# Optimization experiments

Hardware: AMD Instinct MI355X
Metric: run time of the kernel (lower is better)

Reference implementation:

```python
import jax, jax.numpy as jnp
import numpy as np

N = 8192        # nodes
E = 262144      # edges (avg degree 32)
IN_CH = 256
CH = 128
SLOPE = 0.2     # PyG GATv2Conv default negative_slope


def gatv2(x, src, dst, wl, wr, att, b):
    """Single-head GATv2Conv (PyG defaults: share_weights=False, self-loops
    already appended to src/dst). x: [N, in]; wl, wr: [out, in]; att: [out]."""
    xl = x @ wl.T                      # [N, out] source-side transform (x_j)
    xr = x @ wr.T                      # [N, out] target-side transform (x_i)
    # per-edge attention logit: att . LeakyReLU(x_l[src] + x_r[dst])
    e = jax.nn.leaky_relu(xl[src] + xr[dst], SLOPE) @ att   # [E']
    # segment softmax over incoming edges of each target node
    m = jax.ops.segment_max(e, dst, num_segments=N)
    p = jnp.exp(e - m[dst])
    s = jax.ops.segment_sum(p, dst, num_segments=N)
    alpha = p / s[dst]                 # every node has a self-loop -> s > 0
    out = jax.ops.segment_sum(alpha[:, None] * xl[src], dst, num_segments=N)
    return out + b


def setup_inputs() -> dict:
    key = jax.random.key(0)
    ks = jax.random.split(key, 2 + 5 * 3)
    inp = {
        "x": jax.random.normal(ks[0], (N, IN_CH), dtype=jnp.float32),
        "edge_index": jax.random.randint(ks[1], (2, E), 0, N, dtype=jnp.int64),
    }
    dims = [(CH, IN_CH), (2 * CH, CH), (CH, 2 * CH), (CH, 2 * CH), (IN_CH, CH)]
    ki = 2
    for i, (oc, ic) in enumerate(dims, start=1):
        sc = (2.0 / (ic + oc)) ** 0.5  # glorot-ish
        inp[f"w{i}l"] = jax.random.normal(ks[ki], (oc, ic), dtype=jnp.float32) * sc
        inp[f"w{i}r"] = jax.random.normal(ks[ki + 1], (oc, ic), dtype=jnp.float32) * sc
        inp[f"a{i}"] = jax.random.normal(ks[ki + 2], (oc,), dtype=jnp.float32) * sc
        inp[f"b{i}"] = jnp.zeros((oc,), dtype=jnp.float32)
        ki += 3
    return inp


def reference(x, edge_index,
              w1l, w1r, a1, b1,
              w2l, w2r, a2, b2,
              w3l, w3r, a3, b3,
              w4l, w4r, a4, b4,
              w5l, w5r, a5, b5):
    loops = jnp.arange(N, dtype=edge_index.dtype)
    src = jnp.concatenate([edge_index[0], loops])   # add_self_loops=True
    dst = jnp.concatenate([edge_index[1], loops])
    h = jax.nn.relu(gatv2(x, src, dst, w1l, w1r, a1, b1))          # [N, CH]
    z = jax.nn.relu(gatv2(h, src, dst, w2l, w2r, a2, b2))          # [N, 2CH]
    re = jax.nn.relu(gatv2(z, src, dst, w3l, w3r, a3, b3))         # [N, CH]
    recon_edge = jax.nn.sigmoid(re @ re.T)                         # [N, N]
    xd = jax.nn.relu(gatv2(z, src, dst, w4l, w4r, a4, b4))         # [N, CH]
    x_rec = jax.nn.relu(gatv2(xd, src, dst, w5l, w5r, a5, b5))     # [N, IN_CH]
    return recon_edge, x_rec, z
```

## Files before the change

### kernel.cpp

```cpp
#include <hip/hip_runtime.h>
#include <hip/hip_bf16.h>
#include <math.h>

#define N_NODES 8192
#define N_EDGES 262144
#define EP (N_EDGES + N_NODES)
#define SLOPE 0.2f

typedef short bf16x8 __attribute__((ext_vector_type(8)));
typedef short short4v __attribute__((ext_vector_type(4)));
typedef unsigned short u16x8 __attribute__((ext_vector_type(8)));
typedef float f32x4 __attribute__((ext_vector_type(4)));

__global__ void extract_hist(const int* __restrict__ raw,
                             int* __restrict__ esrc, int* __restrict__ edst,
                             int* __restrict__ counts) {
    __shared__ int sflag;
    int t = threadIdx.x;
    if (t < 64) {
        unsigned long long b = __ballot(raw[2 * t + 1] != 0);
        if (t == 0) sflag = (b == 0ULL) ? 1 : 0;
    }
    __syncthreads();
    int i64f = sflag;
    int k = blockIdx.x * blockDim.x + t;
    if (k >= N_EDGES) return;
    int s, d;
    if (i64f) {
        s = raw[2 * (size_t)k];
        d = raw[2 * ((size_t)N_EDGES + k)];
    } else {
        s = raw[k];
        d = raw[N_EDGES + k];
    }
    esrc[k] = s;
    edst[k] = d;
    atomicAdd(&counts[d], 1);
}

__global__ void scan_k(const int* __restrict__ counts, int* __restrict__ row_ptr) {
    __shared__ int part[256];
    int t = threadIdx.x;
    int base = t * 32;
    int loc[32];
    int s = 0;
    for (int i = 0; i < 32; ++i) { loc[i] = s; s += counts[base + i] + 1; }
    part[t] = s;
    __syncthreads();
    for (int off = 1; off < 256; off <<= 1) {
        int tmp = (t >= off) ? part[t - off] : 0;
        __syncthreads();
        part[t] += tmp;
        __syncthreads();
    }
    int incl = part[t];
    int excl = incl - s;
    for (int i = 0; i < 32; ++i) row_ptr[base + i] = excl + loc[i];
    if (t == 255) row_ptr[N_NODES] = incl;
}

__global__ void scatter_k(const int* __restrict__ esrc, const int* __restrict__ edst,
                          const int* __restrict__ row_ptr, int* __restrict__ cursor,
                          int* __restrict__ ssrc) {
    int k = blockIdx.x * blockDim.x + threadIdx.x;
    if (k >= EP) return;
    int s, d;
    if (k < N_EDGES) { s = esrc[k]; d = edst[k]; }
    else             { s = d = k - N_EDGES; }
    int pos = row_ptr[d] + atomicAdd(&cursor[d], 1);
    ssrc[pos] = s;
}

struct WPrep {
    const float* wl[5];
    const float* wr[5];
    int oc[5];
    int lk[5];
};

__global__ void prep_all(WPrep P, const float* __restrict__ x,
                         short* __restrict__ W3all, short* __restrict__ A3) {
    int gid = blockIdx.x * blockDim.x + threadIdx.x;
    if (gid < 524288) {
        int r = gid >> 6;
        int c4 = (gid & 63) << 2;
        f32x4 a = *(const f32x4*)&x[((size_t)r << 8) + c4];
        short4v h4, l4;
#pragma unroll
        for (int j = 0; j < 4; ++j) {
            __hip_bfloat16 hb = __float2bfloat16(a[j]);
            float hf = __bfloat162float(hb);
            __hip_bfloat16 lb = __float2bfloat16(a[j] - hf);
            h4[j] = *(short*)&hb;
            l4[j] = *(short*)&lb;
        }
        size_t ro = (size_t)r * 768;
        *(short4v*)&A3[ro + c4] = h4;
        *(short4v*)&A3[ro + 256 + c4] = l4;
        *(short4v*)&A3[ro + 512 + c4] = h4;
    } else {
        int g = gid - 524288;
        int l = g >> 16;
        if (l >= 5) return;
        int rem = g & 65535;
        int lk = P.lk[l], K = 1 << lk;
        int r = rem >> lk, c = rem & (K - 1);
        int OC = P.oc[l];
        const float* w = (r < OC) ? P.wl[l] : P.wr[l];
        int rr = (r < OC) ? r : r - OC;
        float a = w[((size_t)rr << lk) + c];
        __hip_bfloat16 hb = __float2bfloat16(a);
        float hf = __bfloat162float(hb);
        __hip_bfloat16 lb = __float2bfloat16(a - hf);
        size_t ro = (size_t)l * 196608 + (size_t)r * 3 * K;
        W3all[ro + c] = *(short*)&hb;
        W3all[ro + K + c] = *(short*)&hb;
        W3all[ro + 2 * K + c] = *(short*)&lb;
    }
}

#if __has_builtin(__builtin_amdgcn_global_load_lds)
#define GL16(gsrc, lbase, lofs)                                                       \
    __builtin_amdgcn_global_load_lds((const __attribute__((address_space(1))) void*)(gsrc), \
                                     (__attribute__((address_space(3))) void*)(lbase), 16, 0, 0)
#else
#define GL16(gsrc, lbase, lofs) (*(bf16x8*)((lbase) + (lofs)) = *(const bf16x8*)(gsrc))
#endif

__global__ __launch_bounds__(256) void gemm_bf16_nt(const short* __restrict__ A3,
                                                    const short* __restrict__ W3,
                                                    unsigned short* __restrict__ XLb,
                                                    float* __restrict__ XRf,
                                                    int K3, int N2, int ocl, int lgpl) {
    __shared__ __align__(16) short As[2][4096];
    __shared__ __align__(16) short Bs[2][4096];
    int tid = threadIdx.x;
    int gx = gridDim.x;
    int lgx = (gx == 8) ? 3 : 2;
    int orig = blockIdx.x + (blockIdx.y << lgx);
    int nwg = gx << 7;
    int swzb = (orig & 7) * (nwg >> 3) + (orig >> 3);
    int bx = swzb & (gx - 1), by = swzb >> lgx;
    int i0 = by * 64, j0 = bx * 64;

    int wave = tid >> 6, lane = tid & 63;
    int b0 = wave * 1024 + lane * 16;
    int row0 = b0 >> 7;
    int rb0 = b0 & 127;
    int scb = rb0 ^ ((row0 & 7) << 4);
    const short* gA0 = A3 + (size_t)(i0 + row0) * K3 + (scb >> 1);
    const short* gA1 = A3 + (size_t)(i0 + row0 + 32) * K3 + (scb >> 1);
    const short* gB0 = W3 + (size_t)(j0 + row0) * K3 + (scb >> 1);
    const short* gB1 = W3 + (size_t)(j0 + row0 + 32) * K3 + (scb >> 1);
    int lofs = lane * 8;

#define STAGE(pb, k0s)                                      \
    do {                                                    \
        GL16(gA0 + (k0s), &As[pb][wave * 512], lofs);       \
        GL16(gA1 + (k0s), &As[pb][2048 + wave * 512], lofs);\
        GL16(gB0 + (k0s), &Bs[pb][wave * 512], lofs);       \
        GL16(gB1 + (k0s), &Bs[pb][2048 + wave * 512], lofs);\
    } while (0)

    int wr = (wave >> 1) * 32, wc = (wave & 1) * 32;
    int lm = lane & 15, quad = lane >> 4;
    f32x4 acc[2][2] = {};
    int nt = K3 >> 6;
    STAGE(0, 0);
    int cur = 0;
    for (int t = 0; t < nt; ++t) {
        if (t + 1 < nt) {
            STAGE(cur ^ 1, (t + 1) << 6);
            asm volatile("s_waitcnt vmcnt(4)" ::: "memory");
        } else {
            asm volatile("s_waitcnt vmcnt(0)" ::: "memory");
        }
        __builtin_amdgcn_s_barrier();
        __builtin_amdgcn_sched_barrier(0);
        const char* Ab = (const char*)&As[cur][0];
        const char* Bb = (const char*)&Bs[cur][0];
#pragma unroll
        for (int ks = 0; ks < 2; ++ks) {
            int kb = ks * 64 + quad * 16;
            bf16x8 a[2], b[2];
#pragma unroll
            for (int u = 0; u < 2; ++u) {
                int r = wr + u * 16 + lm;
                a[u] = *(const bf16x8*)(Ab + (((r << 7) | kb) ^ ((r & 7) << 4)));
            }
#pragma unroll
            for (int v = 0; v < 2; ++v) {
                int r = wc + v * 16 + lm;
                b[v] = *(const bf16x8*)(Bb + (((r << 7) | kb) ^ ((r & 7) << 4)));
            }
#pragma unroll
            for (int u = 0; u < 2; ++u)
#pragma unroll
                for (int v = 0; v < 2; ++v)
                    acc[u][v] = __builtin_amdgcn_mfma_f32_16x16x32_bf16(a[u], b[v], acc[u][v], 0, 0, 0);
        }
        __builtin_amdgcn_sched_barrier(0);
        __builtin_amdgcn_s_barrier();
        cur ^= 1;
    }
#undef STAGE
    int plm = (1 << lgpl) - 1;
#pragma unroll
    for (int u = 0; u < 2; ++u)
#pragma unroll
        for (int v = 0; v < 2; ++v)
#pragma unroll
            for (int r = 0; r < 4; ++r) {
                int row = i0 + wr + u * 16 + quad * 4 + r;
                int col = j0 + wc + v * 16 + lm;
                int slab = col >> lgpl;
                int wn = col & plm;
                float val = acc[u][v][r];
                size_t base = (size_t)slab * N_NODES * ocl + (size_t)row * ocl;
                if (wn < ocl) {
                    __hip_bfloat16 hb = __float2bfloat16(val);
                    XLb[base + wn] = *(unsigned short*)&hb;
                } else {
                    XRf[base + wn - ocl] = val;
                }
            }
}

#define LSTR 136

__global__ __launch_bounds__(256) void recon_sym(const unsigned short* __restrict__ Rb,
                                                 float* __restrict__ C) {
    __shared__ __align__(16) short Sh[2 * 128 * LSTR];
    short* As = Sh;
    short* Bs = Sh + 128 * LSTR;
    int tid = threadIdx.x;
    int orig = blockIdx.x;
    int s = (orig & 7) * 260 + (orig >> 3);
    float ff = 64.5f - sqrtf(64.5f * 64.5f - 2.0f * (float)s);
    int bi = (int)ff;
    while (bi > 0 && 64 * bi - bi * (bi - 1) / 2 > s) --bi;
    while (64 * (bi + 1) - (bi + 1) * bi / 2 <= s) ++bi;
    int bj = bi + (s - (64 * bi - bi * (bi - 1) / 2));
    int i0 = bi * 128, j0 = bj * 128;
    const short* R = (const short*)Rb;
#pragma unroll
    for (int c = 0; c < 8; ++c) {
        int idx = tid + c * 256;
        int row = idx >> 4, col = (idx & 15) * 8;
        *(bf16x8*)(&As[row * LSTR + col]) = *(const bf16x8*)(&R[(size_t)(i0 + row) * 128 + col]);
        *(bf16x8*)(&Bs[row * LSTR + col]) = *(const bf16x8*)(&R[(size_t)(j0 + row) * 128 + col]);
    }
    __syncthreads();
    int wave = tid >> 6, lane = tid & 63;
    int wr = (wave >> 1) * 64, wc = (wave & 1) * 64;
    int lm = lane & 15, quad = lane >> 4;
    f32x4 acc[4][4] = {};
#pragma unroll
    for (int ks = 0; ks < 4; ++ks) {
        int ko = ks * 32 + quad * 8;
        bf16x8 a[4], b[4];
#pragma unroll
        for (int u = 0; u < 4; ++u)
            a[u] = *(const bf16x8*)(&As[(wr + u * 16 + lm) * LSTR + ko]);
#pragma unroll
        for (int v = 0; v < 4; ++v)
            b[v] = *(const bf16x8*)(&Bs[(wc + v * 16 + lm) * LSTR + ko]);
#pragma unroll
        for (int u = 0; u < 4; ++u)
#pragma unroll
            for (int v = 0; v < 4; ++v)
                acc[u][v] = __builtin_amdgcn_mfma_f32_16x16x32_bf16(a[u], b[v], acc[u][v], 0, 0, 0);
    }
#pragma unroll
    for (int u = 0; u < 4; ++u)
#pragma unroll
        for (int v = 0; v < 4; ++v)
#pragma unroll
            for (int r = 0; r < 4; ++r) {
                acc[u][v][r] = 1.0f / (1.0f + __expf(-acc[u][v][r]));
                int row = i0 + wr + u * 16 + quad * 4 + r;
                int col = j0 + wc + v * 16 + lm;
                C[(size_t)row * 8192 + col] = acc[u][v][r];
            }
    if (bi != bj) {
        __syncthreads();
        float* T = (float*)Sh;
#pragma unroll
        for (int u = 0; u < 4; ++u)
#pragma unroll
            for (int v = 0; v < 4; ++v)
#pragma unroll
                for (int r = 0; r < 4; ++r)
                    T[(wr + u * 16 + quad * 4 + r) * 129 + (wc + v * 16 + lm)] = acc[u][v][r];
        __syncthreads();
#pragma unroll
        for (int it = 0; it < 64; ++it) {
            int idx = tid + it * 256;
            int rp = idx >> 7, cp = idx & 127;
            C[(size_t)(j0 + rp) * 8192 + (i0 + cp)] = T[cp * 129 + rp];
        }
    }
}

struct GatP {
    const float* att; const float* bias;
    float* outf; short* a3; unsigned short* rb;
    const unsigned short* xlb; const float* xrf;
};

__device__ __forceinline__ void cvt8(u16x8 w, float* v) {
#pragma unroll
    for (int j = 0; j < 8; ++j) v[j] = __uint_as_float(((unsigned)w[j]) << 16);
}

__global__ __launch_bounds__(256) void gat128(const int* __restrict__ row_ptr,
                                              const int* __restrict__ ssrc,
                                              GatP P0, GatP P1) {
    __shared__ float sacc[16][128];
    __shared__ float ss[16];
    int d = blockIdx.x & (N_NODES - 1);
    GatP P = (blockIdx.x >= N_NODES) ? P1 : P0;
    int t = threadIdx.x, ln = t & 15, g = t >> 4;
    int beg = row_ptr[d], end = row_ptr[d + 1];
    float xr[8], at[8];
    {
        f32x4 a0 = *(const f32x4*)&P.xrf[(size_t)d * 128 + ln * 8];
        f32x4 a1 = *(const f32x4*)&P.xrf[(size_t)d * 128 + ln * 8 + 4];
        f32x4 b0 = *(const f32x4*)&P.att[ln * 8];
        f32x4 b1 = *(const f32x4*)&P.att[ln * 8 + 4];
#pragma unroll
        for (int j = 0; j < 4; ++j) { xr[j] = a0[j]; xr[4 + j] = a1[j]; at[j] = b0[j]; at[4 + j] = b1[j]; }
    }
    float s = 0.0f, acc[8] = {};
    int p = beg + g;
    for (; p + 16 < end; p += 32) {
        int s0 = ssrc[p], s1 = ssrc[p + 16];
        float v0[8], v1[8];
        cvt8(*(const u16x8*)&P.xlb[(size_t)s0 * 128 + ln * 8], v0);
        cvt8(*(const u16x8*)&P.xlb[(size_t)s1 * 128 + ln * 8], v1);
        float e0 = 0.0f, e1 = 0.0f;
#pragma unroll
        for (int j = 0; j < 8; ++j) {
            float u0 = v0[j] + xr[j]; u0 = (u0 > 0.0f) ? u0 : SLOPE * u0; e0 += u0 * at[j];
            float u1 = v1[j] + xr[j]; u1 = (u1 > 0.0f) ? u1 : SLOPE * u1; e1 += u1 * at[j];
        }
#pragma unroll
        for (int off = 8; off; off >>= 1) {
            e0 += __shfl_xor(e0, off, 64);
            e1 += __shfl_xor(e1, off, 64);
        }
        float q0 = __expf(e0), q1 = __expf(e1);
        s += q0 + q1;
#pragma unroll
        for (int j = 0; j < 8; ++j) acc[j] += q0 * v0[j] + q1 * v1[j];
    }
    if (p < end) {
        int si = ssrc[p];
        float v[8];
        cvt8(*(const u16x8*)&P.xlb[(size_t)si * 128 + ln * 8], v);
        float e = 0.0f;
#pragma unroll
        for (int j = 0; j < 8; ++j) {
            float u = v[j] + xr[j];
            u = (u > 0.0f) ? u : SLOPE * u;
            e += u * at[j];
        }
#pragma unroll
        for (int off = 8; off; off >>= 1) e += __shfl_xor(e, off, 64);
        float q = __expf(e);
        s += q;
#pragma unroll
        for (int j = 0; j < 8; ++j) acc[j] += q * v[j];
    }
#pragma unroll
    for (int j = 0; j < 8; ++j) sacc[g][ln * 8 + j] = acc[j];
    if (ln == 0) ss[g] = s;
    __syncthreads();
    if (t < 128) {
        float tot = 0.0f, st = 0.0f;
#pragma unroll
        for (int w = 0; w < 16; ++w) { tot += sacc[w][t]; st += ss[w]; }
        float val = fmaxf(tot / st + P.bias[t], 0.0f);
        if (P.outf) P.outf[(size_t)d * 128 + t] = val;
        if (P.a3) {
            __hip_bfloat16 hb = __float2bfloat16(val);
            float hf = __bfloat162float(hb);
            __hip_bfloat16 lb = __float2bfloat16(val - hf);
            size_t ro = (size_t)d * 384;
            P.a3[ro + t] = *(short*)&hb;
            P.a3[ro + 128 + t] = *(short*)&lb;
            P.a3[ro + 256 + t] = *(short*)&hb;
        }
        if (P.rb) {
            __hip_bfloat16 hb = __float2bfloat16(val);
            P.rb[d * 128 + t] = *(unsigned short*)&hb;
        }
    }
}

__global__ __launch_bounds__(256) void gat256(const int* __restrict__ row_ptr,
                                              const int* __restrict__ ssrc,
                                              const unsigned short* __restrict__ xlb,
                                              const float* __restrict__ xrf,
                                              const float* __restrict__ att,
                                              const float* __restrict__ bias,
                                              float* __restrict__ outf,
                                              short* __restrict__ a3) {
    __shared__ float sacc[8][256];
    __shared__ float ss[8];
    int d = blockIdx.x, t = threadIdx.x;
    int ln = t & 31, g = t >> 5;
    int beg = row_ptr[d], end = row_ptr[d + 1];
    float xr[8], at[8];
    {
        f32x4 a0 = *(const f32x4*)&xrf[(size_t)d * 256 + ln * 8];
        f32x4 a1 = *(const f32x4*)&xrf[(size_t)d * 256 + ln * 8 + 4];
        f32x4 b0 = *(const f32x4*)&att[ln * 8];
        f32x4 b1 = *(const f32x4*)&att[ln * 8 + 4];
#pragma unroll
        for (int j = 0; j < 4; ++j) { xr[j] = a0[j]; xr[4 + j] = a1[j]; at[j] = b0[j]; at[4 + j] = b1[j]; }
    }
    float s = 0.0f, acc[8] = {};
    int p = beg + g;
    for (; p + 8 < end; p += 16) {
        int s0 = ssrc[p], s1 = ssrc[p + 8];
        float v0[8], v1[8];
        cvt8(*(const u16x8*)&xlb[(size_t)s0 * 256 + ln * 8], v0);
        cvt8(*(const u16x8*)&xlb[(size_t)s1 * 256 + ln * 8], v1);
        float e0 = 0.0f, e1 = 0.0f;
#pragma unroll
        for (int j = 0; j < 8; ++j) {
            float u0 = v0[j] + xr[j]; u0 = (u0 > 0.0f) ? u0 : SLOPE * u0; e0 += u0 * at[j];
            float u1 = v1[j] + xr[j]; u1 = (u1 > 0.0f) ? u1 : SLOPE * u1; e1 += u1 * at[j];
        }
#pragma unroll
        for (int off = 16; off; off >>= 1) {
            e0 += __shfl_xor(e0, off, 64);
            e1 += __shfl_xor(e1, off, 64);
        }
        float q0 = __expf(e0), q1 = __expf(e1);
        s += q0 + q1;
#pragma unroll
        for (int j = 0; j < 8; ++j) acc[j] += q0 * v0[j] + q1 * v1[j];
    }
    if (p < end) {
        int si = ssrc[p];
        float v[8];
        cvt8(*(const u16x8*)&xlb[(size_t)si * 256 + ln * 8], v);
        float e = 0.0f;
#pragma unroll
        for (int j = 0; j < 8; ++j) {
            float u = v[j] + xr[j];
            u = (u > 0.0f) ? u : SLOPE * u;
            e += u * at[j];
        }
#pragma unroll
        for (int off = 16; off; off >>= 1) e += __shfl_xor(e, off, 64);
        float q = __expf(e);
        s += q;
#pragma unroll
        for (int j = 0; j < 8; ++j) acc[j] += q * v[j];
    }
#pragma unroll
    for (int j = 0; j < 8; ++j) sacc[g][ln * 8 + j] = acc[j];
    if (ln == 0) ss[g] = s;
    __syncthreads();
    {
        float tot = 0.0f, st = 0.0f;
#pragma unroll
        for (int w = 0; w < 8; ++w) { tot += sacc[w][t]; st += ss[w]; }
        float val = fmaxf(tot / st + bias[t], 0.0f);
        if (outf) outf[(size_t)d * 256 + t] = val;
        if (a3) {
            __hip_bfloat16 hb = __float2bfloat16(val);
            float hf = __bfloat162float(hb);
            __hip_bfloat16 lb = __float2bfloat16(val - hf);
            size_t ro = (size_t)d * 768;
            a3[ro + t] = *(short*)&hb;
            a3[ro + 256 + t] = *(short*)&lb;
            a3[ro + 512 + t] = *(short*)&hb;
        }
    }
}

static inline int ceil_div(int a, int b) { return (a + b - 1) / b; }

extern "C" void kernel_launch(void* const* d_in, const int* in_sizes, int n_in,
                              void* d_out, int out_size, void* d_ws, size_t ws_size,
                              hipStream_t stream) {
    const float* x    = (const float*)d_in[0];
    const int*   eraw = (const int*)d_in[1];

    WPrep P;
    const float* att[5];
    const float* bia[5];
    for (int l = 0; l < 5; ++l) {
        P.wl[l] = (const float*)d_in[2 + 4 * l + 0];
        P.wr[l] = (const float*)d_in[2 + 4 * l + 1];
        att[l]  = (const float*)d_in[2 + 4 * l + 2];
        bia[l]  = (const float*)d_in[2 + 4 * l + 3];
    }
    const int och[5]  = {128, 256, 128, 128, 256};
    const int logK[5] = {8, 7, 8, 8, 7};
    for (int l = 0; l < 5; ++l) { P.oc[l] = och[l]; P.lk[l] = logK[l]; }

    float* outp  = (float*)d_out;
    float* recon = outp;
    float* xrec  = outp + (size_t)67108864;
    float* zout  = outp + (size_t)69206016;

    float* W = (float*)d_ws;
    unsigned short* XLb = (unsigned short*)W;
    float* XRf   = W + 1048576;
    short* A3    = (short*)(W + 3145728);
    short* W3all = (short*)(W + 6291456);
    unsigned short* Rb = (unsigned short*)(W + 6782976);
    int* I       = (int*)(W + 7307264);
    int* counts  = I;
    int* cursor  = I + 8192;
    int* row_ptr = I + 16384;
    int* ssrc    = I + 24577;
    int* esrc    = I + 294913;
    int* edst    = I + 557057;

    hipMemsetAsync(counts, 0, 2 * 8192 * sizeof(int), stream);
    extract_hist<<<ceil_div(N_EDGES, 256), 256, 0, stream>>>(eraw, esrc, edst, counts);
    scan_k<<<1, 256, 0, stream>>>(counts, row_ptr);
    scatter_k<<<ceil_div(EP, 256), 256, 0, stream>>>(esrc, edst, row_ptr, cursor, ssrc);

    prep_all<<<3328, 256, 0, stream>>>(P, x, W3all, A3);

    {
        dim3 g(4, 128);
        gemm_bf16_nt<<<g, 256, 0, stream>>>(A3, W3all + 0 * 196608, XLb, XRf, 768, 256, 128, 8);
        GatP g0{att[0], bia[0], nullptr, A3, nullptr, XLb, XRf};
        gat128<<<N_NODES, 256, 0, stream>>>(row_ptr, ssrc, g0, g0);
    }
    {
        dim3 g(8, 128);
        gemm_bf16_nt<<<g, 256, 0, stream>>>(A3, W3all + 1 * 196608, XLb, XRf, 384, 512, 256, 9);
        gat256<<<N_NODES, 256, 0, stream>>>(row_ptr, ssrc, XLb, XRf, att[1], bia[1], zout, A3);
    }
    {
        dim3 g(8, 128);
        gemm_bf16_nt<<<g, 256, 0, stream>>>(A3, W3all + 2 * 196608, XLb, XRf, 768, 512, 128, 8);
        GatP g2{att[2], bia[2], nullptr, nullptr, Rb, XLb, XRf};
        GatP g3{att[3], bia[3], nullptr, A3, nullptr, XLb + (size_t)N_NODES * 128, XRf + (size_t)N_NODES * 128};
        gat128<<<2 * N_NODES, 256, 0, stream>>>(row_ptr, ssrc, g2, g3);
        recon_sym<<<2080, 256, 0, stream>>>(Rb, recon);
    }
    {
        dim3 g(8, 128);
        gemm_bf16_nt<<<g, 256, 0, stream>>>(A3, W3all + 4 * 196608, XLb, XRf, 384, 512, 256, 9);
        gat256<<<N_NODES, 256, 0, stream>>>(row_ptr, ssrc, XLb, XRf, att[4], bia[4], xrec, nullptr);
    }
}
```

Measured before the change: 521.7 us.

## Split recon GEMM into 64-tiles and co-schedule with last-layer GEMM and GAT

The symmetric recon_edge GEMM is rebuilt with 64x64 tiles (8256 upper-triangle tiles) and split into two halves. One half is appended as extra blocks to the layer-5 projection GEMM and the other to the layer-5 GAT kernel, so the store-bound recon work overlaps with those small kernels instead of running alone. Edge histogramming is also folded into the weight/input prep kernel, the separate esrc/edst extraction pass is removed (scatter reads the raw indices), scan stages counts in LDS, and recon stores become nontemporal. The cost is more tile-index arithmetic, larger shared memory per block, and possible load imbalance between heterogeneous blocks.

```diff
diff --git a/kernel.cpp b/kernel.cpp
--- a/kernel.cpp
+++ b/kernel.cpp
@@ -11,65 +11,6 @@
 typedef short short4v __attribute__((ext_vector_type(4)));
 typedef unsigned short u16x8 __attribute__((ext_vector_type(8)));
 typedef float f32x4 __attribute__((ext_vector_type(4)));
-
-__global__ void extract_hist(const int* __restrict__ raw,
-                             int* __restrict__ esrc, int* __restrict__ edst,
-                             int* __restrict__ counts) {
-    __shared__ int sflag;
-    int t = threadIdx.x;
-    if (t < 64) {
-        unsigned long long b = __ballot(raw[2 * t + 1] != 0);
-        if (t == 0) sflag = (b == 0ULL) ? 1 : 0;
-    }
-    __syncthreads();
-    int i64f = sflag;
-    int k = blockIdx.x * blockDim.x + t;
-    if (k >= N_EDGES) return;
-    int s, d;
-    if (i64f) {
-        s = raw[2 * (size_t)k];
-        d = raw[2 * ((size_t)N_EDGES + k)];
-    } else {
-        s = raw[k];
-        d = raw[N_EDGES + k];
-    }
-    esrc[k] = s;
-    edst[k] = d;
-    atomicAdd(&counts[d], 1);
-}
-
-__global__ void scan_k(const int* __restrict__ counts, int* __restrict__ row_ptr) {
-    __shared__ int part[256];
-    int t = threadIdx.x;
-    int base = t * 32;
-    int loc[32];
-    int s = 0;
-    for (int i = 0; i < 32; ++i) { loc[i] = s; s += counts[base + i] + 1; }
-    part[t] = s;
-    __syncthreads();
-    for (int off = 1; off < 256; off <<= 1) {
-        int tmp = (t >= off) ? part[t - off] : 0;
-        __syncthreads();
-        part[t] += tmp;
-        __syncthreads();
-    }
-    int incl = part[t];
-    int excl = incl - s;
-    for (int i = 0; i < 32; ++i) row_ptr[base + i] = excl + loc[i];
-    if (t == 255) row_ptr[N_NODES] = incl;
-}
-
-__global__ void scatter_k(const int* __restrict__ esrc, const int* __restrict__ edst,
-                          const int* __restrict__ row_ptr, int* __restrict__ cursor,
-                          int* __restrict__ ssrc) {
-    int k = blockIdx.x * blockDim.x + threadIdx.x;
-    if (k >= EP) return;
-    int s, d;
-    if (k < N_EDGES) { s = esrc[k]; d = edst[k]; }
-    else             { s = d = k - N_EDGES; }
-    int pos = row_ptr[d] + atomicAdd(&cursor[d], 1);
-    ssrc[pos] = s;
-}
 
 struct WPrep {
     const float* wl[5];
@@ -78,8 +19,10 @@
     int lk[5];
 };
 
-__global__ void prep_all(WPrep P, const float* __restrict__ x,
-                         short* __restrict__ W3all, short* __restrict__ A3) {
+__global__ void prologue(WPrep P, const float* __restrict__ x,
+                         short* __restrict__ W3all, short* __restrict__ A3,
+                         const int* __restrict__ raw, int* __restrict__ counts) {
+    __shared__ int sflag;
     int gid = blockIdx.x * blockDim.x + threadIdx.x;
     if (gid < 524288) {
         int r = gid >> 6;
@@ -98,10 +41,9 @@
         *(short4v*)&A3[ro + c4] = h4;
         *(short4v*)&A3[ro + 256 + c4] = l4;
         *(short4v*)&A3[ro + 512 + c4] = h4;
-    } else {
+    } else if (gid < 851968) {
         int g = gid - 524288;
         int l = g >> 16;
-        if (l >= 5) return;
         int rem = g & 65535;
         int lk = P.lk[l], K = 1 << lk;
         int r = rem >> lk, c = rem & (K - 1);
@@ -116,7 +58,61 @@
         W3all[ro + c] = *(short*)&hb;
         W3all[ro + K + c] = *(short*)&hb;
         W3all[ro + 2 * K + c] = *(short*)&lb;
-    }
+    } else {
+        int t = threadIdx.x;
+        if (t < 64) {
+            unsigned long long b = __ballot(raw[2 * t + 1] != 0);
+            if (t == 0) sflag = (b == 0ULL) ? 1 : 0;
+        }
+        __syncthreads();
+        int k = gid - 851968;
+        int d = sflag ? raw[2 * ((size_t)N_EDGES + k)] : raw[N_EDGES + k];
+        atomicAdd(&counts[d], 1);
+    }
+}
+
+__global__ void scan_k(const int* __restrict__ counts, int* __restrict__ row_ptr) {
+    __shared__ int buf[8192];
+    __shared__ int part[256];
+    int t = threadIdx.x;
+    for (int i = 0; i < 32; ++i) buf[i * 256 + t] = counts[i * 256 + t];
+    __syncthreads();
+    int base = t * 32;
+    int loc[32];
+    int s = 0;
+    for (int i = 0; i < 32; ++i) { loc[i] = s; s += buf[base + i] + 1; }
+    part[t] = s;
+    __syncthreads();
+    for (int off = 1; off < 256; off <<= 1) {
+        int tmp = (t >= off) ? part[t - off] : 0;
+        __syncthreads();
+        part[t] += tmp;
+        __syncthreads();
+    }
+    int incl = part[t];
+    int excl = incl - s;
+    for (int i = 0; i < 32; ++i) row_ptr[base + i] = excl + loc[i];
+    if (t == 255) row_ptr[N_NODES] = incl;
+}
+
+__global__ void scatter_k(const int* __restrict__ raw, const int* __restrict__ row_ptr,
+                          int* __restrict__ cursor, int* __restrict__ ssrc) {
+    __shared__ int sflag;
+    int t = threadIdx.x;
+    if (t < 64) {
+        unsigned long long b = __ballot(raw[2 * t + 1] != 0);
+        if (t == 0) sflag = (b == 0ULL) ? 1 : 0;
+    }
+    __syncthreads();
+    int k = blockIdx.x * blockDim.x + t;
+    if (k >= EP) return;
+    int s, d;
+    if (k < N_EDGES) {
+        if (sflag) { s = raw[2 * (size_t)k]; d = raw[2 * ((size_t)N_EDGES + k)]; }
+        else       { s = raw[k]; d = raw[N_EDGES + k]; }
+    } else s = d = k - N_EDGES;
+    int pos = row_ptr[d] + atomicAdd(&cursor[d], 1);
+    ssrc[pos] = s;
 }
 
 #if __has_builtin(__builtin_amdgcn_global_load_lds)
@@ -127,22 +123,12 @@
 #define GL16(gsrc, lbase, lofs) (*(bf16x8*)((lbase) + (lofs)) = *(const bf16x8*)(gsrc))
 #endif
 
-__global__ __launch_bounds__(256) void gemm_bf16_nt(const short* __restrict__ A3,
-                                                    const short* __restrict__ W3,
-                                                    unsigned short* __restrict__ XLb,
-                                                    float* __restrict__ XRf,
-                                                    int K3, int N2, int ocl, int lgpl) {
-    __shared__ __align__(16) short As[2][4096];
-    __shared__ __align__(16) short Bs[2][4096];
+__device__ __forceinline__ void gemm_body(const short* __restrict__ A3, const short* __restrict__ W3,
+                                          unsigned short* __restrict__ XLb, float* __restrict__ XRf,
+                                          int K3, int ocl, int lgpl,
+                                          int bx, int by, short* SH) {
     int tid = threadIdx.x;
-    int gx = gridDim.x;
-    int lgx = (gx == 8) ? 3 : 2;
-    int orig = blockIdx.x + (blockIdx.y << lgx);
-    int nwg = gx << 7;
-    int swzb = (orig & 7) * (nwg >> 3) + (orig >> 3);
-    int bx = swzb & (gx - 1), by = swzb >> lgx;
     int i0 = by * 64, j0 = bx * 64;
-
     int wave = tid >> 6, lane = tid & 63;
     int b0 = wave * 1024 + lane * 16;
     int row0 = b0 >> 7;
@@ -156,10 +142,12 @@
 
 #define STAGE(pb, k0s)                                      \
     do {                                                    \
-        GL16(gA0 + (k0s), &As[pb][wave * 512], lofs);       \
-        GL16(gA1 + (k0s), &As[pb][2048 + wave * 512], lofs);\
-        GL16(gB0 + (k0s), &Bs[pb][wave * 512], lofs);       \
-        GL16(gB1 + (k0s), &Bs[pb][2048 + wave * 512], lofs);\
+        short* Ad = SH + (pb) * 4096;                       \
+        short* Bd = SH + 8192 + (pb) * 4096;                \
+        GL16(gA0 + (k0s), Ad + wave * 512, lofs);           \
+        GL16(gA1 + (k0s), Ad + 2048 + wave * 512, lofs);    \
+        GL16(gB0 + (k0s), Bd + wave * 512, lofs);           \
+        GL16(gB1 + (k0s), Bd + 2048 + wave * 512, lofs);    \
     } while (0)
 
     int wr = (wave >> 1) * 32, wc = (wave & 1) * 32;
@@ -177,8 +165,8 @@
         }
         __builtin_amdgcn_s_barrier();
         __builtin_amdgcn_sched_barrier(0);
-        const char* Ab = (const char*)&As[cur][0];
-        const char* Bb = (const char*)&Bs[cur][0];
+        const char* Ab = (const char*)(SH + cur * 4096);
+        const char* Bb = (const char*)(SH + 8192 + cur * 4096);
 #pragma unroll
         for (int ks = 0; ks < 2; ++ks) {
             int kb = ks * 64 + quad * 16;
@@ -226,79 +214,109 @@
             }
 }
 
-#define LSTR 136
-
-__global__ __launch_bounds__(256) void recon_sym(const unsigned short* __restrict__ Rb,
-                                                 float* __restrict__ C) {
-    __shared__ __align__(16) short Sh[2 * 128 * LSTR];
-    short* As = Sh;
-    short* Bs = Sh + 128 * LSTR;
+__global__ __launch_bounds__(256) void gemm_std(const short* __restrict__ A3,
+                                                const short* __restrict__ W3,
+                                                unsigned short* __restrict__ XLb,
+                                                float* __restrict__ XRf,
+                                                int K3, int ocl, int lgpl, int lgx) {
+    __shared__ __align__(16) short SH[16384];
+    int nwg = gridDim.x;
+    int orig = blockIdx.x;
+    int swzb = (orig & 7) * (nwg >> 3) + (orig >> 3);
+    int bx = swzb & ((1 << lgx) - 1), by = swzb >> lgx;
+    gemm_body(A3, W3, XLb, XRf, K3, ocl, lgpl, bx, by, SH);
+}
+
+__device__ __forceinline__ void recon64_body(int s, const unsigned short* __restrict__ Rb,
+                                             float* __restrict__ C, short* SH) {
+    float ff = 128.5f - sqrtf(128.5f * 128.5f - 2.0f * (float)s);
+    int bi = (int)ff;
+    if (bi < 0) bi = 0;
+    if (bi > 127) bi = 127;
+    while (bi > 0 && (bi * (257 - bi)) / 2 > s) --bi;
+    while (((bi + 1) * (257 - (bi + 1))) / 2 <= s) ++bi;
+    int bj = bi + (s - (bi * (257 - bi)) / 2);
+    int i0 = bi * 64, j0 = bj * 64;
+    short* As = SH;
+    short* Bs = SH + 64 * 136;
+    const short* R = (const short*)Rb;
     int tid = threadIdx.x;
-    int orig = blockIdx.x;
-    int s = (orig & 7) * 260 + (orig >> 3);
-    float ff = 64.5f - sqrtf(64.5f * 64.5f - 2.0f * (float)s);
-    int bi = (int)ff;
-    while (bi > 0 && 64 * bi - bi * (bi - 1) / 2 > s) --bi;
-    while (64 * (bi + 1) - (bi + 1) * bi / 2 <= s) ++bi;
-    int bj = bi + (s - (64 * bi - bi * (bi - 1) / 2));
-    int i0 = bi * 128, j0 = bj * 128;
-    const short* R = (const short*)Rb;
-#pragma unroll
-    for (int c = 0; c < 8; ++c) {
+#pragma unroll
+    for (int c = 0; c < 4; ++c) {
         int idx = tid + c * 256;
         int row = idx >> 4, col = (idx & 15) * 8;
-        *(bf16x8*)(&As[row * LSTR + col]) = *(const bf16x8*)(&R[(size_t)(i0 + row) * 128 + col]);
-        *(bf16x8*)(&Bs[row * LSTR + col]) = *(const bf16x8*)(&R[(size_t)(j0 + row) * 128 + col]);
+        *(bf16x8*)(&As[row * 136 + col]) = *(const bf16x8*)(&R[(size_t)(i0 + row) * 128 + col]);
+        *(bf16x8*)(&Bs[row * 136 + col]) = *(const bf16x8*)(&R[(size_t)(j0 + row) * 128 + col]);
     }
     __syncthreads();
     int wave = tid >> 6, lane = tid & 63;
-    int wr = (wave >> 1) * 64, wc = (wave & 1) * 64;
+    int wr = (wave >> 1) * 32, wc = (wave & 1) * 32;
     int lm = lane & 15, quad = lane >> 4;
-    f32x4 acc[4][4] = {};
+    f32x4 acc[2][2] = {};
 #pragma unroll
     for (int ks = 0; ks < 4; ++ks) {
         int ko = ks * 32 + quad * 8;
-        bf16x8 a[4], b[4];
-#pragma unroll
-        for (int u = 0; u < 4; ++u)
-            a[u] = *(const bf16x8*)(&As[(wr + u * 16 + lm) * LSTR + ko]);
-#pragma unroll
-        for (int v = 0; v < 4; ++v)
-            b[v] = *(const bf16x8*)(&Bs[(wc + v * 16 + lm) * LSTR + ko]);
-#pragma unroll
-        for (int u = 0; u < 4; ++u)
-#pragma unroll
-            for (int v = 0; v < 4; ++v)
+        bf16x8 a[2], b[2];
+#pragma unroll
+        for (int u = 0; u < 2; ++u)
+            a[u] = *(const bf16x8*)(&As[(wr + u * 16 + lm) * 136 + ko]);
+#pragma unroll
+        for (int v = 0; v < 2; ++v)
+            b[v] = *(const bf16x8*)(&Bs[(wc + v * 16 + lm) * 136 + ko]);
+#pragma unroll
+        for (int u = 0; u < 2; ++u)
+#pragma unroll
+            for (int v = 0; v < 2; ++v)
                 acc[u][v] = __builtin_amdgcn_mfma_f32_16x16x32_bf16(a[u], b[v], acc[u][v], 0, 0, 0);
     }
 #pragma unroll
-    for (int u = 0; u < 4; ++u)
-#pragma unroll
-        for (int v = 0; v < 4; ++v)
+    for (int u = 0; u < 2; ++u)
+#pragma unroll
+        for (int v = 0; v < 2; ++v)
 #pragma unroll
             for (int r = 0; r < 4; ++r) {
-                acc[u][v][r] = 1.0f / (1.0f + __expf(-acc[u][v][r]));
+                float sg = 1.0f / (1.0f + __expf(-acc[u][v][r]));
+                acc[u][v][r] = sg;
                 int row = i0 + wr + u * 16 + quad * 4 + r;
                 int col = j0 + wc + v * 16 + lm;
-                C[(size_t)row * 8192 + col] = acc[u][v][r];
+                __builtin_nontemporal_store(sg, &C[(size_t)row * 8192 + col]);
             }
     if (bi != bj) {
         __syncthreads();
-        float* T = (float*)Sh;
-#pragma unroll
-        for (int u = 0; u < 4; ++u)
-#pragma unroll
-            for (int v = 0; v < 4; ++v)
+        float* T = (float*)SH;
+#pragma unroll
+        for (int u = 0; u < 2; ++u)
+#pragma unroll
+            for (int v = 0; v < 2; ++v)
 #pragma unroll
                 for (int r = 0; r < 4; ++r)
-                    T[(wr + u * 16 + quad * 4 + r) * 129 + (wc + v * 16 + lm)] = acc[u][v][r];
+                    T[(wr + u * 16 + quad * 4 + r) * 65 + (wc + v * 16 + lm)] = acc[u][v][r];
         __syncthreads();
 #pragma unroll
-        for (int it = 0; it < 64; ++it) {
+        for (int it = 0; it < 16; ++it) {
             int idx = tid + it * 256;
-            int rp = idx >> 7, cp = idx & 127;
-            C[(size_t)(j0 + rp) * 8192 + (i0 + cp)] = T[cp * 129 + rp];
-        }
+            int rp = idx >> 6, cp = idx & 63;
+            __builtin_nontemporal_store(T[cp * 65 + rp], &C[(size_t)(j0 + rp) * 8192 + (i0 + cp)]);
+        }
+    }
+}
+
+__global__ __launch_bounds__(256) void gemm_recon(const short* __restrict__ A3,
+                                                  const short* __restrict__ W3,
+                                                  unsigned short* __restrict__ XLb,
+                                                  float* __restrict__ XRf,
+                                                  int K3, int ocl, int lgpl,
+                                                  const unsigned short* __restrict__ Rb,
+                                                  float* __restrict__ C, int sbase) {
+    __shared__ __align__(16) short SH[17408];
+    int id = blockIdx.x;
+    if (id < 1024) {
+        int swzb = (id & 7) * 128 + (id >> 3);
+        gemm_body(A3, W3, XLb, XRf, K3, ocl, lgpl, swzb & 7, swzb >> 3, SH);
+    } else {
+        int orig = id - 1024;
+        int s = (orig & 7) * 516 + (orig >> 3) + sbase;
+        recon64_body(s, Rb, C, SH);
     }
 }
 
@@ -398,17 +416,16 @@
     }
 }
 
-__global__ __launch_bounds__(256) void gat256(const int* __restrict__ row_ptr,
-                                              const int* __restrict__ ssrc,
-                                              const unsigned short* __restrict__ xlb,
-                                              const float* __restrict__ xrf,
-                                              const float* __restrict__ att,
-                                              const float* __restrict__ bias,
-                                              float* __restrict__ outf,
-                                              short* __restrict__ a3) {
-    __shared__ float sacc[8][256];
-    __shared__ float ss[8];
-    int d = blockIdx.x, t = threadIdx.x;
+__device__ __forceinline__ void gat256_body(const int* __restrict__ row_ptr,
+                                            const int* __restrict__ ssrc,
+                                            const unsigned short* __restrict__ xlb,
+                                            const float* __restrict__ xrf,
+                                            const float* __restrict__ att,
+                                            const float* __restrict__ bias,
+                                            float* __restrict__ outf,
+                                            short* __restrict__ a3,
+                                            int d, float* sacc, float* ss) {
+    int t = threadIdx.x;
     int ln = t & 31, g = t >> 5;
     int beg = row_ptr[d], end = row_ptr[d + 1];
     float xr[8], at[8];
@@ -462,13 +479,13 @@
         for (int j = 0; j < 8; ++j) acc[j] += q * v[j];
     }
 #pragma unroll
-    for (int j = 0; j < 8; ++j) sacc[g][ln * 8 + j] = acc[j];
+    for (int j = 0; j < 8; ++j) sacc[g * 256 + ln * 8 + j] = acc[j];
     if (ln == 0) ss[g] = s;
     __syncthreads();
     {
         float tot = 0.0f, st = 0.0f;
 #pragma unroll
-        for (int w = 0; w < 8; ++w) { tot += sacc[w][t]; st += ss[w]; }
+        for (int w = 0; w < 8; ++w) { tot += sacc[w * 256 + t]; st += ss[w]; }
         float val = fmaxf(tot / st + bias[t], 0.0f);
         if (outf) outf[(size_t)d * 256 + t] = val;
         if (a3) {
@@ -480,6 +497,39 @@
             a3[ro + 256 + t] = *(short*)&lb;
             a3[ro + 512 + t] = *(short*)&hb;
         }
+    }
+}
+
+__global__ __launch_bounds__(256) void gat256(const int* __restrict__ row_ptr,
+                                              const int* __restrict__ ssrc,
+                                              const unsigned short* __restrict__ xlb,
+                                              const float* __restrict__ xrf,
+                                              const float* __restrict__ att,
+                                              const float* __restrict__ bias,
+                                              float* __restrict__ outf,
+                                              short* __restrict__ a3) {
+    __shared__ float SA[8 * 256 + 8];
+    gat256_body(row_ptr, ssrc, xlb, xrf, att, bias, outf, a3, blockIdx.x, SA, SA + 8 * 256);
+}
+
+__global__ __launch_bounds__(256) void gat256_recon(const int* __restrict__ row_ptr,
+                                                    const int* __restrict__ ssrc,
+                                                    const unsigned short* __restrict__ xlb,
+                                                    const float* __restrict__ xrf,
+                                                    const float* __restrict__ att,
+                                                    const float* __restrict__ bias,
+                                                    float* __restrict__ outf,
+                                                    const unsigned short* __restrict__ Rb,
+                                                    float* __restrict__ C, int sbase) {
+    __shared__ __align__(16) short SH[17408];
+    int id = blockIdx.x;
+    if (id < N_NODES) {
+        float* SA = (float*)SH;
+        gat256_body(row_ptr, ssrc, xlb, xrf, att, bias, outf, nullptr, id, SA, SA + 8 * 256);
+    } else {
+        int orig = id - N_NODES;
+        int s = (orig & 7) * 516 + (orig >> 3) + sbase;
+        recon64_body(s, Rb, C, SH);
     }
 }
 
@@ -520,38 +570,29 @@
     int* cursor  = I + 8192;
     int* row_ptr = I + 16384;
     int* ssrc    = I + 24577;
-    int* esrc    = I + 294913;
-    int* edst    = I + 557057;
 
     hipMemsetAsync(counts, 0, 2 * 8192 * sizeof(int), stream);
-    extract_hist<<<ceil_div(N_EDGES, 256), 256, 0, stream>>>(eraw, esrc, edst, counts);
+    prologue<<<4352, 256, 0, stream>>>(P, x, W3all, A3, eraw, counts);
     scan_k<<<1, 256, 0, stream>>>(counts, row_ptr);
-    scatter_k<<<ceil_div(EP, 256), 256, 0, stream>>>(esrc, edst, row_ptr, cursor, ssrc);
-
-    prep_all<<<3328, 256, 0, stream>>>(P, x, W3all, A3);
+    scatter_k<<<ceil_div(EP, 256), 256, 0, stream>>>(eraw, row_ptr, cursor, ssrc);
 
     {
-        dim3 g(4, 128);
-        gemm_bf16_nt<<<g, 256, 0, stream>>>(A3, W3all + 0 * 196608, XLb, XRf, 768, 256, 128, 8);
+        gemm_std<<<512, 256, 0, stream>>>(A3, W3all + 0 * 196608, XLb, XRf, 768, 128, 8, 2);
         GatP g0{att[0], bia[0], nullptr, A3, nullptr, XLb, XRf};
         gat128<<<N_NODES, 256, 0, stream>>>(row_ptr, ssrc, g0, g0);
     }
     {
-        dim3 g(8, 128);
-        gemm_bf16_nt<<<g, 256, 0, stream>>>(A3, W3all + 1 * 196608, XLb, XRf, 384, 512, 256, 9);
+        gemm_std<<<1024, 256, 0, stream>>>(A3, W3all + 1 * 196608, XLb, XRf, 384, 256, 9, 3);
         gat256<<<N_NODES, 256, 0, stream>>>(row_ptr, ssrc, XLb, XRf, att[1], bia[1], zout, A3);
     }
     {
-        dim3 g(8, 128);
-        gemm_bf16_nt<<<g, 256, 0, stream>>>(A3, W3all + 2 * 196608, XLb, XRf, 768, 512, 128, 8);
+        gemm_std<<<1024, 256, 0, stream>>>(A3, W3all + 2 * 196608, XLb, XRf, 768, 128, 8, 3);
         GatP g2{att[2], bia[2], nullptr, nullptr, Rb, XLb, XRf};
         GatP g3{att[3], bia[3], nullptr, A3, nullptr, XLb + (size_t)N_NODES * 128, XRf + (size_t)N_NODES * 128};
         gat128<<<2 * N_NODES, 256, 0, stream>>>(row_ptr, ssrc, g2, g3);
-        recon_sym<<<2080, 256, 0, stream>>>(Rb, recon);
-    }
-    {
-        dim3 g(8, 128);
-        gemm_bf16_nt<<<g, 256, 0, stream>>>(A3, W3all + 4 * 196608, XLb, XRf, 384, 512, 256, 9);
-        gat256<<<N_NODES, 256, 0, stream>>>(row_ptr, ssrc, XLb, XRf, att[4], bia[4], xrec, nullptr);
-    }
-}
+    }
+    gemm_recon<<<1024 + 4128, 256, 0, stream>>>(A3, W3all + 4 * 196608, XLb, XRf, 384, 256, 9,
+                                                Rb, recon, 0);
+    gat256_recon<<<N_NODES + 4128, 256, 0, stream>>>(row_ptr, ssrc, XLb, XRf, att[4], bia[4],
+                                                     xrec, Rb, recon, 4128);
+}
```

Result: no change. 523.1 us (+0.3%).
